# Optimization experiments

Measured on AMD Instinct MI355X. Metric: run time of the kernel, lower is better.

Reference implementation:

```python
import jax, jax.numpy as jnp
import numpy as np

N_NODE = 8192
H1 = 512
R_EMB = 128
N_EDGE = 262144
N_REG = 2048


def gcn_conv(x, W, b, src, dst, n):
    """PyG-style GCNConv: add self-loops, sym-normalize, linear, scatter-add."""
    h = x @ W  # [n, out]
    loop = jnp.arange(n)
    src2 = jnp.concatenate([src, loop])
    dst2 = jnp.concatenate([dst, loop])
    ones = jnp.ones(src2.shape[0], dtype=h.dtype)
    deg = jax.ops.segment_sum(ones, dst2, num_segments=n)  # in-degree incl. self-loop
    dis = jnp.where(deg > 0, jax.lax.rsqrt(deg), 0.0)
    norm = dis[src2] * dis[dst2]  # [E+n]
    msg = h[src2] * norm[:, None]  # gather + scale
    return jax.ops.segment_sum(msg, dst2, num_segments=n) + b


def setup_inputs() -> dict:
    key = jax.random.key(0)
    k1, k2, k3, k4 = jax.random.split(key, 4)
    edge_index = jax.random.randint(k1, (N_EDGE, 2), 0, N_NODE)  # [E,2] (src,dst) pairs
    reg_id = jax.random.randint(k2, (N_REG,), 0, N_NODE)
    W1 = jax.random.normal(k3, (N_NODE, H1), dtype=jnp.float32) * 0.02
    b1 = jnp.zeros((H1,), dtype=jnp.float32)
    W2 = jax.random.normal(k4, (H1, R_EMB), dtype=jnp.float32) * 0.02
    b2 = jnp.zeros((R_EMB,), dtype=jnp.float32)
    return {"reg_id": reg_id, "edge_index": edge_index, "W1": W1, "b1": b1, "W2": W2, "b2": b2}


def reference(reg_id, edge_index, W1, b1, W2, b2):
    src = edge_index[:, 0]
    dst = edge_index[:, 1]
    n = W1.shape[0]
    x = jnp.eye(n, dtype=W1.dtype)  # identity feature matrix (one-hot per node)
    h = jax.nn.relu(gcn_conv(x, W1, b1, src, dst, n))
    # dropout is identity at inference
    out = gcn_conv(h, W2, b2, src, dst, n)  # [n, R_EMB]
    return out[reg_id]
```

## Files before the change

kernel.cpp:

```cpp
#include <hip/hip_runtime.h>
#include <hip/hip_bf16.h>

typedef unsigned int u32;

#define N_NODE 8192
#define H1 512
#define R_EMB 128
#define N_EDGE 262144
#define N_REG 2048

#define OFF_DEG        (0)
#define OFF_ROWSTART   (64 * 1024)
#define OFF_CURSOR     (128 * 1024)
#define OFF_DIS        (160 * 1024)
#define OFF_SORTED     (256 * 1024)
#define OFF_W1S        (2 * 1024 * 1024)
#define OFF_H1S        (10 * 1024 * 1024)
#define OFF_W2T        (18 * 1024 * 1024)
#define OFF_G          (19 * 1024 * 1024)

__device__ inline u32 rne_bf16(float f) {
    u32 u = __float_as_uint(f);
    u += 0x7fffu + ((u >> 16) & 1u);
    return u >> 16;
}
__device__ inline float bf_lo(u32 u) { return __uint_as_float(u << 16); }
__device__ inline float bf_hi(u32 u) { return __uint_as_float(u & 0xffff0000u); }

using frag_ab = __attribute__((ext_vector_type(8))) short;
using frag_cd = __attribute__((ext_vector_type(4))) float;

#define ACC8(v, q) \
    v##0 += bf_lo(q.x); v##1 += bf_hi(q.x); \
    v##2 += bf_lo(q.y); v##3 += bf_hi(q.y); \
    v##4 += bf_lo(q.z); v##5 += bf_hi(q.z); \
    v##6 += bf_lo(q.w); v##7 += bf_hi(q.w);

__global__ void hist_kernel(const int* __restrict__ edge, int* __restrict__ deg) {
    int e = blockIdx.x * blockDim.x + threadIdx.x;
    if (e < N_EDGE) {
        int dst = edge[2 * e + 1];
        atomicAdd(&deg[dst], 1);
    }
}

__global__ void scan_kernel(const int* __restrict__ deg, int* __restrict__ row_start,
                            int* __restrict__ cursor, float* __restrict__ dis) {
    __shared__ int wtot[16];
    __shared__ int wpre[16];
    int t = threadIdx.x;
    int lane = t & 63;
    int wv = t >> 6;
    int base = t * 8;
    int local[8];
    int sum = 0;
#pragma unroll
    for (int j = 0; j < 8; j++) {
        local[j] = deg[base + j];
        sum += local[j];
    }
    int sc = sum;
#pragma unroll
    for (int off = 1; off < 64; off <<= 1) {
        int y = __shfl_up(sc, off, 64);
        if (lane >= off) sc += y;
    }
    if (lane == 63) wtot[wv] = sc;
    __syncthreads();
    if (wv == 0 && lane < 16) {
        int v = wtot[lane];
        int s2 = v;
#pragma unroll
        for (int off = 1; off < 16; off <<= 1) {
            int y = __shfl_up(s2, off, 64);
            if (lane >= off) s2 += y;
        }
        wpre[lane] = s2 - v;
    }
    __syncthreads();
    int run = wpre[wv] + (sc - sum);
#pragma unroll
    for (int j = 0; j < 8; j++) {
        row_start[base + j] = run;
        cursor[base + j] = run;
        dis[base + j] = rsqrtf((float)(local[j] + 1));
        run += local[j];
    }
    if (t == 1023) row_start[N_NODE] = run;
}

__global__ void prep_kernel(const int* __restrict__ edge, int* __restrict__ cursor,
                            int* __restrict__ sorted_src,
                            const float* __restrict__ W1, const float* __restrict__ dis,
                            u32* __restrict__ W1s,
                            const float* __restrict__ W2, u32* __restrict__ w2t) {
    int bid = blockIdx.x;
    if (bid < 1024) {
        int e = bid * 256 + threadIdx.x;
        int src = edge[2 * e + 0];
        int dst = edge[2 * e + 1];
        int pos = atomicAdd(&cursor[dst], 1);
        sorted_src[pos] = src;
    } else if (bid < 1024 + 8192) {
        int idx = (bid - 1024) * 256 + threadIdx.x;
        int row = idx >> 8;
        int pc = idx & 255;
        float d = dis[row];
        float2 f = *(const float2*)(W1 + ((size_t)row << 9) + (pc << 1));
        W1s[idx] = rne_bf16(f.x * d) | (rne_bf16(f.y * d) << 16);
    } else {
        int idx = (bid - 9216) * 256 + threadIdx.x;
        int j = idx >> 8;
        int p = idx & 255;
        float a = W2[(size_t)(2 * p) * R_EMB + j];
        float b = W2[(size_t)(2 * p + 1) * R_EMB + j];
        w2t[idx] = rne_bf16(a) | (rne_bf16(b) << 16);
    }
}

__global__ void layer1_kernel(const u32* __restrict__ W1s, const float* __restrict__ b1,
                              const int* __restrict__ row_start, const int* __restrict__ sorted_src,
                              const float* __restrict__ dis, u32* __restrict__ h1s) {
    int d = blockIdx.x * 4 + (threadIdx.x >> 6);
    int t = threadIdx.x & 63;
    float disd = dis[d];
    const uint4* base = (const uint4*)W1s;

    uint4 wd = base[(d << 6) + t];
    float a0 = bf_lo(wd.x), a1 = bf_hi(wd.x), a2 = bf_lo(wd.y), a3 = bf_hi(wd.y);
    float a4 = bf_lo(wd.z), a5 = bf_hi(wd.z), a6 = bf_lo(wd.w), a7 = bf_hi(wd.w);
    float c0 = 0, c1 = 0, c2 = 0, c3 = 0, c4 = 0, c5 = 0, c6 = 0, c7 = 0;

    int beg = row_start[d], end = row_start[d + 1];
    int n = end - beg;
    int i = beg;
    int rem = n & 3;
    for (int r = 0; r < rem; r++) {
        int s = sorted_src[i++];
        uint4 v0 = base[(s << 6) + t];
        ACC8(a, v0)
    }
    for (; i < end; i += 4) {
        int s0 = sorted_src[i];
        int s1 = sorted_src[i + 1];
        int s2 = sorted_src[i + 2];
        int s3 = sorted_src[i + 3];
        uint4 v0 = base[(s0 << 6) + t];
        uint4 v1 = base[(s1 << 6) + t];
        uint4 v2 = base[(s2 << 6) + t];
        uint4 v3 = base[(s3 << 6) + t];
        ACC8(a, v0)
        ACC8(c, v1)
        ACC8(a, v2)
        ACC8(c, v3)
    }
    a0 += c0; a1 += c1; a2 += c2; a3 += c3;
    a4 += c4; a5 += c5; a6 += c6; a7 += c7;

    int f = t * 8;
    float4 bl = *(const float4*)(b1 + f);
    float4 bh = *(const float4*)(b1 + f + 4);
    float o0 = fmaxf(a0 * disd + bl.x, 0.0f) * disd;
    float o1 = fmaxf(a1 * disd + bl.y, 0.0f) * disd;
    float o2 = fmaxf(a2 * disd + bl.z, 0.0f) * disd;
    float o3 = fmaxf(a3 * disd + bl.w, 0.0f) * disd;
    float o4 = fmaxf(a4 * disd + bh.x, 0.0f) * disd;
    float o5 = fmaxf(a5 * disd + bh.y, 0.0f) * disd;
    float o6 = fmaxf(a6 * disd + bh.z, 0.0f) * disd;
    float o7 = fmaxf(a7 * disd + bh.w, 0.0f) * disd;
    uint4 o;
    o.x = rne_bf16(o0) | (rne_bf16(o1) << 16);
    o.y = rne_bf16(o2) | (rne_bf16(o3) << 16);
    o.z = rne_bf16(o4) | (rne_bf16(o5) << 16);
    o.w = rne_bf16(o6) | (rne_bf16(o7) << 16);
    ((uint4*)h1s)[(d << 6) + t] = o;
}

__global__ void layer2_agg_kernel(const u32* __restrict__ h1s, const int* __restrict__ reg_id,
                                  const int* __restrict__ row_start, const int* __restrict__ sorted_src,
                                  const float* __restrict__ dis, u32* __restrict__ g_bf) {
    int tgt = blockIdx.x * 4 + (threadIdx.x >> 6);
    int d = reg_id[tgt];
    int t = threadIdx.x & 63;
    float disd = dis[d];
    const uint4* base = (const uint4*)h1s;

    uint4 wd = base[(d << 6) + t];
    float a0 = bf_lo(wd.x), a1 = bf_hi(wd.x), a2 = bf_lo(wd.y), a3 = bf_hi(wd.y);
    float a4 = bf_lo(wd.z), a5 = bf_hi(wd.z), a6 = bf_lo(wd.w), a7 = bf_hi(wd.w);
    float c0 = 0, c1 = 0, c2 = 0, c3 = 0, c4 = 0, c5 = 0, c6 = 0, c7 = 0;

    int beg = row_start[d], end = row_start[d + 1];
    int n = end - beg;
    int i = beg;
    int rem = n & 3;
    for (int r = 0; r < rem; r++) {
        int s = sorted_src[i++];
        uint4 v0 = base[(s << 6) + t];
        ACC8(a, v0)
    }
    for (; i < end; i += 4) {
        int s0 = sorted_src[i];
        int s1 = sorted_src[i + 1];
        int s2 = sorted_src[i + 2];
        int s3 = sorted_src[i + 3];
        uint4 v0 = base[(s0 << 6) + t];
        uint4 v1 = base[(s1 << 6) + t];
        uint4 v2 = base[(s2 << 6) + t];
        uint4 v3 = base[(s3 << 6) + t];
        ACC8(a, v0)
        ACC8(c, v1)
        ACC8(a, v2)
        ACC8(c, v3)
    }
    a0 += c0; a1 += c1; a2 += c2; a3 += c3;
    a4 += c4; a5 += c5; a6 += c6; a7 += c7;

    uint4 o;
    o.x = rne_bf16(a0 * disd) | (rne_bf16(a1 * disd) << 16);
    o.y = rne_bf16(a2 * disd) | (rne_bf16(a3 * disd) << 16);
    o.z = rne_bf16(a4 * disd) | (rne_bf16(a5 * disd) << 16);
    o.w = rne_bf16(a6 * disd) | (rne_bf16(a7 * disd) << 16);
    ((uint4*)g_bf)[(tgt << 6) + t] = o;
}

__global__ void gemm_out_mfma(const u32* __restrict__ g_bf, const u32* __restrict__ w2t_bf,
                              const float* __restrict__ b2, float* __restrict__ out) {
    int w = blockIdx.x * 4 + (threadIdx.x >> 6);
    int lane = threadIdx.x & 63;
    int tm = w >> 3;
    int tn = w & 7;
    int r15 = lane & 15;
    int kb4 = (lane >> 4) << 2;

    const uint4* arow = (const uint4*)(g_bf + ((tm * 16 + r15) << 8) + kb4);
    const uint4* brow = (const uint4*)(w2t_bf + ((tn * 16 + r15) << 8) + kb4);
    frag_cd acc = {0.0f, 0.0f, 0.0f, 0.0f};
#pragma unroll
    for (int kk = 0; kk < 16; kk++) {
        uint4 av = arow[kk * 4];
        uint4 bv = brow[kk * 4];
        acc = __builtin_amdgcn_mfma_f32_16x16x32_bf16(*(frag_ab*)&av, *(frag_ab*)&bv, acc, 0, 0, 0);
    }
    int col = tn * 16 + r15;
    int row0 = tm * 16 + ((lane >> 4) << 2);
    float bias = b2[col];
#pragma unroll
    for (int r = 0; r < 4; r++)
        out[(size_t)(row0 + r) * R_EMB + col] = acc[r] + bias;
}

extern "C" void kernel_launch(void* const* d_in, const int* in_sizes, int n_in,
                              void* d_out, int out_size, void* d_ws, size_t ws_size,
                              hipStream_t stream) {
    const int* reg_id = (const int*)d_in[0];
    const int* edge = (const int*)d_in[1];
    const float* W1 = (const float*)d_in[2];
    const float* b1 = (const float*)d_in[3];
    const float* W2 = (const float*)d_in[4];
    const float* b2 = (const float*)d_in[5];
    float* out = (float*)d_out;

    char* ws = (char*)d_ws;
    int* deg = (int*)(ws + OFF_DEG);
    int* row_start = (int*)(ws + OFF_ROWSTART);
    int* cursor = (int*)(ws + OFF_CURSOR);
    float* dis = (float*)(ws + OFF_DIS);
    int* sorted_src = (int*)(ws + OFF_SORTED);
    u32* W1s = (u32*)(ws + OFF_W1S);
    u32* h1s = (u32*)(ws + OFF_H1S);
    u32* w2t = (u32*)(ws + OFF_W2T);
    u32* g_bf = (u32*)(ws + OFF_G);

    hipMemsetAsync(deg, 0, N_NODE * sizeof(int), stream);

    hist_kernel<<<N_EDGE / 256, 256, 0, stream>>>(edge, deg);
    scan_kernel<<<1, 1024, 0, stream>>>(deg, row_start, cursor, dis);
    prep_kernel<<<1024 + 8192 + 128, 256, 0, stream>>>(edge, cursor, sorted_src,
                                                       W1, dis, W1s, W2, w2t);
    layer1_kernel<<<N_NODE / 4, 256, 0, stream>>>(W1s, b1, row_start, sorted_src, dis, h1s);
    layer2_agg_kernel<<<N_REG / 4, 256, 0, stream>>>(h1s, reg_id, row_start, sorted_src, dis, g_bf);
    gemm_out_mfma<<<256, 256, 0, stream>>>(g_bf, w2t, b2, out);
}
```

Baseline: 150.3 us.

## Stage feature-column chunks in LDS for both aggregation layers

W1 and h1 are now stored column-chunked, as 64 chunks of 8 bf16 features per node, so that one 128 KB chunk fits in LDS. Each block loads one chunk into shared memory and gathers neighbour rows from LDS instead of global memory, with one thread per destination node. This replaces scattered global gathers with LDS reads. In exchange it adds per-block tile load traffic, lowers occupancy (128 KB LDS per block, only 256 blocks), and leaves threads load-imbalanced by node degree, with strided sorted_src reads.

```diff
diff --git a/kernel.cpp b/kernel.cpp
--- a/kernel.cpp
+++ b/kernel.cpp
@@ -14,8 +14,8 @@
 #define OFF_CURSOR     (128 * 1024)
 #define OFF_DIS        (160 * 1024)
 #define OFF_SORTED     (256 * 1024)
-#define OFF_W1S        (2 * 1024 * 1024)
-#define OFF_H1S        (10 * 1024 * 1024)
+#define OFF_W1C        (2 * 1024 * 1024)
+#define OFF_H1C        (10 * 1024 * 1024)
 #define OFF_W2T        (18 * 1024 * 1024)
 #define OFF_G          (19 * 1024 * 1024)
 
@@ -92,7 +92,7 @@
 __global__ void prep_kernel(const int* __restrict__ edge, int* __restrict__ cursor,
                             int* __restrict__ sorted_src,
                             const float* __restrict__ W1, const float* __restrict__ dis,
-                            u32* __restrict__ W1s,
+                            uint4* __restrict__ W1c,
                             const float* __restrict__ W2, u32* __restrict__ w2t) {
     int bid = blockIdx.x;
     if (bid < 1024) {
@@ -101,15 +101,22 @@
         int dst = edge[2 * e + 1];
         int pos = atomicAdd(&cursor[dst], 1);
         sorted_src[pos] = src;
-    } else if (bid < 1024 + 8192) {
+    } else if (bid < 3072) {
         int idx = (bid - 1024) * 256 + threadIdx.x;
-        int row = idx >> 8;
-        int pc = idx & 255;
+        int row = idx & 8191;
+        int c = idx >> 13;
         float d = dis[row];
-        float2 f = *(const float2*)(W1 + ((size_t)row << 9) + (pc << 1));
-        W1s[idx] = rne_bf16(f.x * d) | (rne_bf16(f.y * d) << 16);
+        const float* p = W1 + ((size_t)row << 9) + (c << 3);
+        float4 f0 = *(const float4*)p;
+        float4 f1 = *(const float4*)(p + 4);
+        uint4 o;
+        o.x = rne_bf16(f0.x * d) | (rne_bf16(f0.y * d) << 16);
+        o.y = rne_bf16(f0.z * d) | (rne_bf16(f0.w * d) << 16);
+        o.z = rne_bf16(f1.x * d) | (rne_bf16(f1.y * d) << 16);
+        o.w = rne_bf16(f1.z * d) | (rne_bf16(f1.w * d) << 16);
+        W1c[(c << 13) + row] = o;
     } else {
-        int idx = (bid - 9216) * 256 + threadIdx.x;
+        int idx = (bid - 3072) * 256 + threadIdx.x;
         int j = idx >> 8;
         int p = idx & 255;
         float a = W2[(size_t)(2 * p) * R_EMB + j];
@@ -118,110 +125,126 @@
     }
 }
 
-__global__ void layer1_kernel(const u32* __restrict__ W1s, const float* __restrict__ b1,
-                              const int* __restrict__ row_start, const int* __restrict__ sorted_src,
-                              const float* __restrict__ dis, u32* __restrict__ h1s) {
-    int d = blockIdx.x * 4 + (threadIdx.x >> 6);
-    int t = threadIdx.x & 63;
-    float disd = dis[d];
-    const uint4* base = (const uint4*)W1s;
-
-    uint4 wd = base[(d << 6) + t];
-    float a0 = bf_lo(wd.x), a1 = bf_hi(wd.x), a2 = bf_lo(wd.y), a3 = bf_hi(wd.y);
-    float a4 = bf_lo(wd.z), a5 = bf_hi(wd.z), a6 = bf_lo(wd.w), a7 = bf_hi(wd.w);
-    float c0 = 0, c1 = 0, c2 = 0, c3 = 0, c4 = 0, c5 = 0, c6 = 0, c7 = 0;
-
-    int beg = row_start[d], end = row_start[d + 1];
-    int n = end - beg;
-    int i = beg;
-    int rem = n & 3;
-    for (int r = 0; r < rem; r++) {
-        int s = sorted_src[i++];
-        uint4 v0 = base[(s << 6) + t];
-        ACC8(a, v0)
-    }
-    for (; i < end; i += 4) {
-        int s0 = sorted_src[i];
-        int s1 = sorted_src[i + 1];
-        int s2 = sorted_src[i + 2];
-        int s3 = sorted_src[i + 3];
-        uint4 v0 = base[(s0 << 6) + t];
-        uint4 v1 = base[(s1 << 6) + t];
-        uint4 v2 = base[(s2 << 6) + t];
-        uint4 v3 = base[(s3 << 6) + t];
-        ACC8(a, v0)
-        ACC8(c, v1)
-        ACC8(a, v2)
-        ACC8(c, v3)
-    }
-    a0 += c0; a1 += c1; a2 += c2; a3 += c3;
-    a4 += c4; a5 += c5; a6 += c6; a7 += c7;
-
-    int f = t * 8;
-    float4 bl = *(const float4*)(b1 + f);
-    float4 bh = *(const float4*)(b1 + f + 4);
-    float o0 = fmaxf(a0 * disd + bl.x, 0.0f) * disd;
-    float o1 = fmaxf(a1 * disd + bl.y, 0.0f) * disd;
-    float o2 = fmaxf(a2 * disd + bl.z, 0.0f) * disd;
-    float o3 = fmaxf(a3 * disd + bl.w, 0.0f) * disd;
-    float o4 = fmaxf(a4 * disd + bh.x, 0.0f) * disd;
-    float o5 = fmaxf(a5 * disd + bh.y, 0.0f) * disd;
-    float o6 = fmaxf(a6 * disd + bh.z, 0.0f) * disd;
-    float o7 = fmaxf(a7 * disd + bh.w, 0.0f) * disd;
-    uint4 o;
-    o.x = rne_bf16(o0) | (rne_bf16(o1) << 16);
-    o.y = rne_bf16(o2) | (rne_bf16(o3) << 16);
-    o.z = rne_bf16(o4) | (rne_bf16(o5) << 16);
-    o.w = rne_bf16(o6) | (rne_bf16(o7) << 16);
-    ((uint4*)h1s)[(d << 6) + t] = o;
-}
-
-__global__ void layer2_agg_kernel(const u32* __restrict__ h1s, const int* __restrict__ reg_id,
-                                  const int* __restrict__ row_start, const int* __restrict__ sorted_src,
-                                  const float* __restrict__ dis, u32* __restrict__ g_bf) {
-    int tgt = blockIdx.x * 4 + (threadIdx.x >> 6);
-    int d = reg_id[tgt];
-    int t = threadIdx.x & 63;
-    float disd = dis[d];
-    const uint4* base = (const uint4*)h1s;
-
-    uint4 wd = base[(d << 6) + t];
-    float a0 = bf_lo(wd.x), a1 = bf_hi(wd.x), a2 = bf_lo(wd.y), a3 = bf_hi(wd.y);
-    float a4 = bf_lo(wd.z), a5 = bf_hi(wd.z), a6 = bf_lo(wd.w), a7 = bf_hi(wd.w);
-    float c0 = 0, c1 = 0, c2 = 0, c3 = 0, c4 = 0, c5 = 0, c6 = 0, c7 = 0;
-
-    int beg = row_start[d], end = row_start[d + 1];
-    int n = end - beg;
-    int i = beg;
-    int rem = n & 3;
-    for (int r = 0; r < rem; r++) {
-        int s = sorted_src[i++];
-        uint4 v0 = base[(s << 6) + t];
-        ACC8(a, v0)
-    }
-    for (; i < end; i += 4) {
-        int s0 = sorted_src[i];
-        int s1 = sorted_src[i + 1];
-        int s2 = sorted_src[i + 2];
-        int s3 = sorted_src[i + 3];
-        uint4 v0 = base[(s0 << 6) + t];
-        uint4 v1 = base[(s1 << 6) + t];
-        uint4 v2 = base[(s2 << 6) + t];
-        uint4 v3 = base[(s3 << 6) + t];
-        ACC8(a, v0)
-        ACC8(c, v1)
-        ACC8(a, v2)
-        ACC8(c, v3)
-    }
-    a0 += c0; a1 += c1; a2 += c2; a3 += c3;
-    a4 += c4; a5 += c5; a6 += c6; a7 += c7;
-
-    uint4 o;
-    o.x = rne_bf16(a0 * disd) | (rne_bf16(a1 * disd) << 16);
-    o.y = rne_bf16(a2 * disd) | (rne_bf16(a3 * disd) << 16);
-    o.z = rne_bf16(a4 * disd) | (rne_bf16(a5 * disd) << 16);
-    o.w = rne_bf16(a6 * disd) | (rne_bf16(a7 * disd) << 16);
-    ((uint4*)g_bf)[(tgt << 6) + t] = o;
+__global__ __launch_bounds__(256) void layer1_lds(const uint4* __restrict__ W1c,
+                                                  const float* __restrict__ b1,
+                                                  const int* __restrict__ row_start,
+                                                  const int* __restrict__ sorted_src,
+                                                  const float* __restrict__ dis,
+                                                  uint4* __restrict__ h1c) {
+    __shared__ uint4 tile[N_NODE];
+    int c = blockIdx.x & 63;
+    int grp = blockIdx.x >> 6;
+    const uint4* src = W1c + (c << 13);
+    for (int k = threadIdx.x; k < N_NODE; k += 256) tile[k] = src[k];
+    __syncthreads();
+
+    float4 bl = *(const float4*)(b1 + (c << 3));
+    float4 bh = *(const float4*)(b1 + (c << 3) + 4);
+
+    for (int m = 0; m < 8; m++) {
+        int d = (grp << 11) + (m << 8) + threadIdx.x;
+        float disd = dis[d];
+        uint4 wd = tile[d];
+        float a0 = bf_lo(wd.x), a1 = bf_hi(wd.x), a2 = bf_lo(wd.y), a3 = bf_hi(wd.y);
+        float a4 = bf_lo(wd.z), a5 = bf_hi(wd.z), a6 = bf_lo(wd.w), a7 = bf_hi(wd.w);
+        float c0 = 0, c1 = 0, c2 = 0, c3 = 0, c4 = 0, c5 = 0, c6 = 0, c7 = 0;
+
+        int beg = row_start[d], end = row_start[d + 1];
+        int i = beg;
+        int rem = (end - beg) & 3;
+        for (int r = 0; r < rem; r++) {
+            int s = sorted_src[i++];
+            uint4 v0 = tile[s];
+            ACC8(a, v0)
+        }
+        for (; i < end; i += 4) {
+            int s0 = sorted_src[i];
+            int s1 = sorted_src[i + 1];
+            int s2 = sorted_src[i + 2];
+            int s3 = sorted_src[i + 3];
+            uint4 v0 = tile[s0];
+            uint4 v1 = tile[s1];
+            uint4 v2 = tile[s2];
+            uint4 v3 = tile[s3];
+            ACC8(a, v0)
+            ACC8(c, v1)
+            ACC8(a, v2)
+            ACC8(c, v3)
+        }
+        a0 += c0; a1 += c1; a2 += c2; a3 += c3;
+        a4 += c4; a5 += c5; a6 += c6; a7 += c7;
+
+        float o0 = fmaxf(a0 * disd + bl.x, 0.0f) * disd;
+        float o1 = fmaxf(a1 * disd + bl.y, 0.0f) * disd;
+        float o2 = fmaxf(a2 * disd + bl.z, 0.0f) * disd;
+        float o3 = fmaxf(a3 * disd + bl.w, 0.0f) * disd;
+        float o4 = fmaxf(a4 * disd + bh.x, 0.0f) * disd;
+        float o5 = fmaxf(a5 * disd + bh.y, 0.0f) * disd;
+        float o6 = fmaxf(a6 * disd + bh.z, 0.0f) * disd;
+        float o7 = fmaxf(a7 * disd + bh.w, 0.0f) * disd;
+        uint4 o;
+        o.x = rne_bf16(o0) | (rne_bf16(o1) << 16);
+        o.y = rne_bf16(o2) | (rne_bf16(o3) << 16);
+        o.z = rne_bf16(o4) | (rne_bf16(o5) << 16);
+        o.w = rne_bf16(o6) | (rne_bf16(o7) << 16);
+        h1c[(c << 13) + d] = o;
+    }
+}
+
+__global__ __launch_bounds__(256) void layer2_lds(const uint4* __restrict__ h1c,
+                                                  const int* __restrict__ reg_id,
+                                                  const int* __restrict__ row_start,
+                                                  const int* __restrict__ sorted_src,
+                                                  const float* __restrict__ dis,
+                                                  uint4* __restrict__ g_bf) {
+    __shared__ uint4 tile[N_NODE];
+    int c = blockIdx.x & 63;
+    int grp = blockIdx.x >> 6;
+    const uint4* src = h1c + (c << 13);
+    for (int k = threadIdx.x; k < N_NODE; k += 256) tile[k] = src[k];
+    __syncthreads();
+
+    for (int m = 0; m < 2; m++) {
+        int tgt = (grp << 9) + (m << 8) + threadIdx.x;
+        int d = reg_id[tgt];
+        float disd = dis[d];
+        uint4 wd = tile[d];
+        float a0 = bf_lo(wd.x), a1 = bf_hi(wd.x), a2 = bf_lo(wd.y), a3 = bf_hi(wd.y);
+        float a4 = bf_lo(wd.z), a5 = bf_hi(wd.z), a6 = bf_lo(wd.w), a7 = bf_hi(wd.w);
+        float c0 = 0, c1 = 0, c2 = 0, c3 = 0, c4 = 0, c5 = 0, c6 = 0, c7 = 0;
+
+        int beg = row_start[d], end = row_start[d + 1];
+        int i = beg;
+        int rem = (end - beg) & 3;
+        for (int r = 0; r < rem; r++) {
+            int s = sorted_src[i++];
+            uint4 v0 = tile[s];
+            ACC8(a, v0)
+        }
+        for (; i < end; i += 4) {
+            int s0 = sorted_src[i];
+            int s1 = sorted_src[i + 1];
+            int s2 = sorted_src[i + 2];
+            int s3 = sorted_src[i + 3];
+            uint4 v0 = tile[s0];
+            uint4 v1 = tile[s1];
+            uint4 v2 = tile[s2];
+            uint4 v3 = tile[s3];
+            ACC8(a, v0)
+            ACC8(c, v1)
+            ACC8(a, v2)
+            ACC8(c, v3)
+        }
+        a0 += c0; a1 += c1; a2 += c2; a3 += c3;
+        a4 += c4; a5 += c5; a6 += c6; a7 += c7;
+
+        uint4 o;
+        o.x = rne_bf16(a0 * disd) | (rne_bf16(a1 * disd) << 16);
+        o.y = rne_bf16(a2 * disd) | (rne_bf16(a3 * disd) << 16);
+        o.z = rne_bf16(a4 * disd) | (rne_bf16(a5 * disd) << 16);
+        o.w = rne_bf16(a6 * disd) | (rne_bf16(a7 * disd) << 16);
+        g_bf[(tgt << 6) + c] = o;
+    }
 }
 
 __global__ void gemm_out_mfma(const u32* __restrict__ g_bf, const u32* __restrict__ w2t_bf,
@@ -267,18 +290,17 @@
     int* cursor = (int*)(ws + OFF_CURSOR);
     float* dis = (float*)(ws + OFF_DIS);
     int* sorted_src = (int*)(ws + OFF_SORTED);
-    u32* W1s = (u32*)(ws + OFF_W1S);
-    u32* h1s = (u32*)(ws + OFF_H1S);
+    uint4* W1c = (uint4*)(ws + OFF_W1C);
+    uint4* h1c = (uint4*)(ws + OFF_H1C);
     u32* w2t = (u32*)(ws + OFF_W2T);
-    u32* g_bf = (u32*)(ws + OFF_G);
+    uint4* g_bf = (uint4*)(ws + OFF_G);
 
     hipMemsetAsync(deg, 0, N_NODE * sizeof(int), stream);
 
     hist_kernel<<<N_EDGE / 256, 256, 0, stream>>>(edge, deg);
     scan_kernel<<<1, 1024, 0, stream>>>(deg, row_start, cursor, dis);
-    prep_kernel<<<1024 + 8192 + 128, 256, 0, stream>>>(edge, cursor, sorted_src,
-                                                       W1, dis, W1s, W2, w2t);
-    layer1_kernel<<<N_NODE / 4, 256, 0, stream>>>(W1s, b1, row_start, sorted_src, dis, h1s);
-    layer2_agg_kernel<<<N_REG / 4, 256, 0, stream>>>(h1s, reg_id, row_start, sorted_src, dis, g_bf);
-    gemm_out_mfma<<<256, 256, 0, stream>>>(g_bf, w2t, b2, out);
-}
+    prep_kernel<<<3200, 256, 0, stream>>>(edge, cursor, sorted_src, W1, dis, W1c, W2, w2t);
+    layer1_lds<<<256, 256, 0, stream>>>(W1c, b1, row_start, sorted_src, dis, h1c);
+    layer2_lds<<<256, 256, 0, stream>>>(h1c, reg_id, row_start, sorted_src, dis, g_bf);
+    gemm_out_mfma<<<256, 256, 0, stream>>>((const u32*)g_bf, w2t, b2, out);
+}
```

New measurement: 177.6 us. 18.2% more time.

## Split hidden features into two halves so each layer-1 gather pass fits in cache

Applied to the files above, without the earlier changes.

W1 scaled bf16 and h1 are now stored as two separate feature halves of 256 columns each. Layer 1 runs one pass per half, so the randomly gathered working set per pass is 4 MB instead of 8 MB and is more likely to stay in L2/MALL. Each lane gathers 8-byte instead of 16-byte chunks, which means more, smaller memory requests. The prep kernel also switches to float4 loads, and layer 2 reads from both halves.

```diff
diff --git a/kernel.cpp b/kernel.cpp
--- a/kernel.cpp
+++ b/kernel.cpp
@@ -14,10 +14,12 @@
 #define OFF_CURSOR     (128 * 1024)
 #define OFF_DIS        (160 * 1024)
 #define OFF_SORTED     (256 * 1024)
-#define OFF_W1S        (2 * 1024 * 1024)
-#define OFF_H1S        (10 * 1024 * 1024)
+#define OFF_W1H        (2 * 1024 * 1024)
+#define OFF_H1H        (10 * 1024 * 1024)
 #define OFF_W2T        (18 * 1024 * 1024)
 #define OFF_G          (19 * 1024 * 1024)
+
+#define HALF_U32 (N_NODE * 128)
 
 __device__ inline u32 rne_bf16(float f) {
     u32 u = __float_as_uint(f);
@@ -30,11 +32,9 @@
 using frag_ab = __attribute__((ext_vector_type(8))) short;
 using frag_cd = __attribute__((ext_vector_type(4))) float;
 
-#define ACC8(v, q) \
+#define ACC4(v, q) \
     v##0 += bf_lo(q.x); v##1 += bf_hi(q.x); \
-    v##2 += bf_lo(q.y); v##3 += bf_hi(q.y); \
-    v##4 += bf_lo(q.z); v##5 += bf_hi(q.z); \
-    v##6 += bf_lo(q.w); v##7 += bf_hi(q.w);
+    v##2 += bf_lo(q.y); v##3 += bf_hi(q.y);
 
 __global__ void hist_kernel(const int* __restrict__ edge, int* __restrict__ deg) {
     int e = blockIdx.x * blockDim.x + threadIdx.x;
@@ -92,7 +92,7 @@
 __global__ void prep_kernel(const int* __restrict__ edge, int* __restrict__ cursor,
                             int* __restrict__ sorted_src,
                             const float* __restrict__ W1, const float* __restrict__ dis,
-                            u32* __restrict__ W1s,
+                            u32* __restrict__ W1h,
                             const float* __restrict__ W2, u32* __restrict__ w2t) {
     int bid = blockIdx.x;
     if (bid < 1024) {
@@ -101,15 +101,19 @@
         int dst = edge[2 * e + 1];
         int pos = atomicAdd(&cursor[dst], 1);
         sorted_src[pos] = src;
-    } else if (bid < 1024 + 8192) {
+    } else if (bid < 5120) {
         int idx = (bid - 1024) * 256 + threadIdx.x;
-        int row = idx >> 8;
-        int pc = idx & 255;
+        int j2 = idx & 63;
+        int row = (idx >> 6) & 8191;
+        int h = idx >> 19;
         float d = dis[row];
-        float2 f = *(const float2*)(W1 + ((size_t)row << 9) + (pc << 1));
-        W1s[idx] = rne_bf16(f.x * d) | (rne_bf16(f.y * d) << 16);
+        float4 f = *(const float4*)(W1 + ((size_t)row << 9) + (h << 8) + (j2 << 2));
+        uint2 o;
+        o.x = rne_bf16(f.x * d) | (rne_bf16(f.y * d) << 16);
+        o.y = rne_bf16(f.z * d) | (rne_bf16(f.w * d) << 16);
+        *(uint2*)(W1h + ((size_t)h * HALF_U32) + (row << 7) + (j2 << 1)) = o;
     } else {
-        int idx = (bid - 9216) * 256 + threadIdx.x;
+        int idx = (bid - 5120) * 256 + threadIdx.x;
         int j = idx >> 8;
         int p = idx & 255;
         float a = W2[(size_t)(2 * p) * R_EMB + j];
@@ -118,110 +122,111 @@
     }
 }
 
-__global__ void layer1_kernel(const u32* __restrict__ W1s, const float* __restrict__ b1,
-                              const int* __restrict__ row_start, const int* __restrict__ sorted_src,
-                              const float* __restrict__ dis, u32* __restrict__ h1s) {
-    int d = blockIdx.x * 4 + (threadIdx.x >> 6);
-    int t = threadIdx.x & 63;
+__global__ __launch_bounds__(256) void layer1_half(const u32* __restrict__ W1h,
+                                                   const float* __restrict__ b1,
+                                                   const int* __restrict__ row_start,
+                                                   const int* __restrict__ sorted_src,
+                                                   const float* __restrict__ dis,
+                                                   u32* __restrict__ h1h) {
+    int half = blockIdx.x >> 11;
+    int d = ((blockIdx.x & 2047) << 2) + (threadIdx.x >> 6);
+    int lane = threadIdx.x & 63;
+    const u32* basep = W1h + (size_t)half * HALF_U32;
+    int loff = lane << 1;
     float disd = dis[d];
-    const uint4* base = (const uint4*)W1s;
-
-    uint4 wd = base[(d << 6) + t];
+
+    uint2 wd = *(const uint2*)(basep + (d << 7) + loff);
     float a0 = bf_lo(wd.x), a1 = bf_hi(wd.x), a2 = bf_lo(wd.y), a3 = bf_hi(wd.y);
-    float a4 = bf_lo(wd.z), a5 = bf_hi(wd.z), a6 = bf_lo(wd.w), a7 = bf_hi(wd.w);
-    float c0 = 0, c1 = 0, c2 = 0, c3 = 0, c4 = 0, c5 = 0, c6 = 0, c7 = 0;
+    float c0 = 0, c1 = 0, c2 = 0, c3 = 0;
 
     int beg = row_start[d], end = row_start[d + 1];
-    int n = end - beg;
     int i = beg;
-    int rem = n & 3;
+    int rem = (end - beg) & 3;
     for (int r = 0; r < rem; r++) {
         int s = sorted_src[i++];
-        uint4 v0 = base[(s << 6) + t];
-        ACC8(a, v0)
+        uint2 v0 = *(const uint2*)(basep + (s << 7) + loff);
+        ACC4(a, v0)
     }
     for (; i < end; i += 4) {
         int s0 = sorted_src[i];
         int s1 = sorted_src[i + 1];
         int s2 = sorted_src[i + 2];
         int s3 = sorted_src[i + 3];
-        uint4 v0 = base[(s0 << 6) + t];
-        uint4 v1 = base[(s1 << 6) + t];
-        uint4 v2 = base[(s2 << 6) + t];
-        uint4 v3 = base[(s3 << 6) + t];
-        ACC8(a, v0)
-        ACC8(c, v1)
-        ACC8(a, v2)
-        ACC8(c, v3)
+        uint2 v0 = *(const uint2*)(basep + (s0 << 7) + loff);
+        uint2 v1 = *(const uint2*)(basep + (s1 << 7) + loff);
+        uint2 v2 = *(const uint2*)(basep + (s2 << 7) + loff);
+        uint2 v3 = *(const uint2*)(basep + (s3 << 7) + loff);
+        ACC4(a, v0)
+        ACC4(c, v1)
+        ACC4(a, v2)
+        ACC4(c, v3)
+    }
+    a0 += c0; a1 += c1; a2 += c2; a3 += c3;
+
+    float4 bb = *(const float4*)(b1 + (half << 8) + (lane << 2));
+    float o0 = fmaxf(a0 * disd + bb.x, 0.0f) * disd;
+    float o1 = fmaxf(a1 * disd + bb.y, 0.0f) * disd;
+    float o2 = fmaxf(a2 * disd + bb.z, 0.0f) * disd;
+    float o3 = fmaxf(a3 * disd + bb.w, 0.0f) * disd;
+    uint2 o;
+    o.x = rne_bf16(o0) | (rne_bf16(o1) << 16);
+    o.y = rne_bf16(o2) | (rne_bf16(o3) << 16);
+    *(uint2*)(h1h + (size_t)half * HALF_U32 + (d << 7) + loff) = o;
+}
+
+__global__ __launch_bounds__(256) void layer2_agg(const u32* __restrict__ h1h,
+                                                  const int* __restrict__ reg_id,
+                                                  const int* __restrict__ row_start,
+                                                  const int* __restrict__ sorted_src,
+                                                  const float* __restrict__ dis,
+                                                  u32* __restrict__ g_bf) {
+    int tgt = (blockIdx.x << 2) + (threadIdx.x >> 6);
+    int lane = threadIdx.x & 63;
+    int d = reg_id[tgt];
+    int loff = lane << 1;
+    float disd = dis[d];
+    const u32* base0 = h1h;
+    const u32* base1 = h1h + HALF_U32;
+
+    uint2 wl = *(const uint2*)(base0 + (d << 7) + loff);
+    uint2 wh = *(const uint2*)(base1 + (d << 7) + loff);
+    float a0 = bf_lo(wl.x), a1 = bf_hi(wl.x), a2 = bf_lo(wl.y), a3 = bf_hi(wl.y);
+    float a4 = bf_lo(wh.x), a5 = bf_hi(wh.x), a6 = bf_lo(wh.y), a7 = bf_hi(wh.y);
+    float c0 = 0, c1 = 0, c2 = 0, c3 = 0, c4 = 0, c5 = 0, c6 = 0, c7 = 0;
+
+    int beg = row_start[d], end = row_start[d + 1];
+    int i = beg;
+    if ((end - beg) & 1) {
+        int s = sorted_src[i++];
+        uint2 v0 = *(const uint2*)(base0 + (s << 7) + loff);
+        uint2 v1 = *(const uint2*)(base1 + (s << 7) + loff);
+        ACC4(a, v0)
+        float t4 = bf_lo(v1.x), t5 = bf_hi(v1.x), t6 = bf_lo(v1.y), t7 = bf_hi(v1.y);
+        a4 += t4; a5 += t5; a6 += t6; a7 += t7;
+    }
+    for (; i < end; i += 2) {
+        int s0 = sorted_src[i];
+        int s1 = sorted_src[i + 1];
+        uint2 v0 = *(const uint2*)(base0 + (s0 << 7) + loff);
+        uint2 v1 = *(const uint2*)(base1 + (s0 << 7) + loff);
+        uint2 v2 = *(const uint2*)(base0 + (s1 << 7) + loff);
+        uint2 v3 = *(const uint2*)(base1 + (s1 << 7) + loff);
+        ACC4(a, v0)
+        a4 += bf_lo(v1.x); a5 += bf_hi(v1.x); a6 += bf_lo(v1.y); a7 += bf_hi(v1.y);
+        ACC4(c, v2)
+        c4 += bf_lo(v3.x); c5 += bf_hi(v3.x); c6 += bf_lo(v3.y); c7 += bf_hi(v3.y);
     }
     a0 += c0; a1 += c1; a2 += c2; a3 += c3;
     a4 += c4; a5 += c5; a6 += c6; a7 += c7;
 
-    int f = t * 8;
-    float4 bl = *(const float4*)(b1 + f);
-    float4 bh = *(const float4*)(b1 + f + 4);
-    float o0 = fmaxf(a0 * disd + bl.x, 0.0f) * disd;
-    float o1 = fmaxf(a1 * disd + bl.y, 0.0f) * disd;
-    float o2 = fmaxf(a2 * disd + bl.z, 0.0f) * disd;
-    float o3 = fmaxf(a3 * disd + bl.w, 0.0f) * disd;
-    float o4 = fmaxf(a4 * disd + bh.x, 0.0f) * disd;
-    float o5 = fmaxf(a5 * disd + bh.y, 0.0f) * disd;
-    float o6 = fmaxf(a6 * disd + bh.z, 0.0f) * disd;
-    float o7 = fmaxf(a7 * disd + bh.w, 0.0f) * disd;
-    uint4 o;
-    o.x = rne_bf16(o0) | (rne_bf16(o1) << 16);
-    o.y = rne_bf16(o2) | (rne_bf16(o3) << 16);
-    o.z = rne_bf16(o4) | (rne_bf16(o5) << 16);
-    o.w = rne_bf16(o6) | (rne_bf16(o7) << 16);
-    ((uint4*)h1s)[(d << 6) + t] = o;
-}
-
-__global__ void layer2_agg_kernel(const u32* __restrict__ h1s, const int* __restrict__ reg_id,
-                                  const int* __restrict__ row_start, const int* __restrict__ sorted_src,
-                                  const float* __restrict__ dis, u32* __restrict__ g_bf) {
-    int tgt = blockIdx.x * 4 + (threadIdx.x >> 6);
-    int d = reg_id[tgt];
-    int t = threadIdx.x & 63;
-    float disd = dis[d];
-    const uint4* base = (const uint4*)h1s;
-
-    uint4 wd = base[(d << 6) + t];
-    float a0 = bf_lo(wd.x), a1 = bf_hi(wd.x), a2 = bf_lo(wd.y), a3 = bf_hi(wd.y);
-    float a4 = bf_lo(wd.z), a5 = bf_hi(wd.z), a6 = bf_lo(wd.w), a7 = bf_hi(wd.w);
-    float c0 = 0, c1 = 0, c2 = 0, c3 = 0, c4 = 0, c5 = 0, c6 = 0, c7 = 0;
-
-    int beg = row_start[d], end = row_start[d + 1];
-    int n = end - beg;
-    int i = beg;
-    int rem = n & 3;
-    for (int r = 0; r < rem; r++) {
-        int s = sorted_src[i++];
-        uint4 v0 = base[(s << 6) + t];
-        ACC8(a, v0)
-    }
-    for (; i < end; i += 4) {
-        int s0 = sorted_src[i];
-        int s1 = sorted_src[i + 1];
-        int s2 = sorted_src[i + 2];
-        int s3 = sorted_src[i + 3];
-        uint4 v0 = base[(s0 << 6) + t];
-        uint4 v1 = base[(s1 << 6) + t];
-        uint4 v2 = base[(s2 << 6) + t];
-        uint4 v3 = base[(s3 << 6) + t];
-        ACC8(a, v0)
-        ACC8(c, v1)
-        ACC8(a, v2)
-        ACC8(c, v3)
-    }
-    a0 += c0; a1 += c1; a2 += c2; a3 += c3;
-    a4 += c4; a5 += c5; a6 += c6; a7 += c7;
-
-    uint4 o;
-    o.x = rne_bf16(a0 * disd) | (rne_bf16(a1 * disd) << 16);
-    o.y = rne_bf16(a2 * disd) | (rne_bf16(a3 * disd) << 16);
-    o.z = rne_bf16(a4 * disd) | (rne_bf16(a5 * disd) << 16);
-    o.w = rne_bf16(a6 * disd) | (rne_bf16(a7 * disd) << 16);
-    ((uint4*)g_bf)[(tgt << 6) + t] = o;
+    uint2 ol, oh;
+    ol.x = rne_bf16(a0 * disd) | (rne_bf16(a1 * disd) << 16);
+    ol.y = rne_bf16(a2 * disd) | (rne_bf16(a3 * disd) << 16);
+    oh.x = rne_bf16(a4 * disd) | (rne_bf16(a5 * disd) << 16);
+    oh.y = rne_bf16(a6 * disd) | (rne_bf16(a7 * disd) << 16);
+    u32* grow = g_bf + ((size_t)tgt << 8);
+    *(uint2*)(grow + loff) = ol;
+    *(uint2*)(grow + 128 + loff) = oh;
 }
 
 __global__ void gemm_out_mfma(const u32* __restrict__ g_bf, const u32* __restrict__ w2t_bf,
@@ -267,8 +272,8 @@
     int* cursor = (int*)(ws + OFF_CURSOR);
     float* dis = (float*)(ws + OFF_DIS);
     int* sorted_src = (int*)(ws + OFF_SORTED);
-    u32* W1s = (u32*)(ws + OFF_W1S);
-    u32* h1s = (u32*)(ws + OFF_H1S);
+    u32* W1h = (u32*)(ws + OFF_W1H);
+    u32* h1h = (u32*)(ws + OFF_H1H);
     u32* w2t = (u32*)(ws + OFF_W2T);
     u32* g_bf = (u32*)(ws + OFF_G);
 
@@ -276,9 +281,8 @@
 
     hist_kernel<<<N_EDGE / 256, 256, 0, stream>>>(edge, deg);
     scan_kernel<<<1, 1024, 0, stream>>>(deg, row_start, cursor, dis);
-    prep_kernel<<<1024 + 8192 + 128, 256, 0, stream>>>(edge, cursor, sorted_src,
-                                                       W1, dis, W1s, W2, w2t);
-    layer1_kernel<<<N_NODE / 4, 256, 0, stream>>>(W1s, b1, row_start, sorted_src, dis, h1s);
-    layer2_agg_kernel<<<N_REG / 4, 256, 0, stream>>>(h1s, reg_id, row_start, sorted_src, dis, g_bf);
+    prep_kernel<<<5248, 256, 0, stream>>>(edge, cursor, sorted_src, W1, dis, W1h, W2, w2t);
+    layer1_half<<<4096, 256, 0, stream>>>(W1h, b1, row_start, sorted_src, dis, h1h);
+    layer2_agg<<<N_REG / 4, 256, 0, stream>>>(h1h, reg_id, row_start, sorted_src, dis, g_bf);
     gemm_out_mfma<<<256, 256, 0, stream>>>(g_bf, w2t, b2, out);
 }
```

Measured after the change: 155.3 us. +3.3%, slower.
